# Performance work log

Measured on AMD Instinct MI355X. Metric: run time of the kernel, lower is better.

Reference implementation:

```python
import jax, jax.numpy as jnp
import numpy as np

NUM_NODES = 50000
NUM_EDGES = 800000
NUM_GRAPHS = 100
NODES_PER_GRAPH = 500
K = 250  # ceil(0.5 * NODES_PER_GRAPH), TopKPooling ratio=0.5
D = 64
OUT = 10


def gcn_conv(x, edge_index, W, b, num_nodes):
    """PyG GCNConv: add self-loops, symmetric D^-1/2 (A+I) D^-1/2 (x @ W) + b."""
    h = x @ W  # [N, Dout]
    loop = jnp.arange(num_nodes)
    row = jnp.concatenate([edge_index[0], loop])  # sources
    col = jnp.concatenate([edge_index[1], loop])  # targets
    deg = jax.ops.segment_sum(jnp.ones_like(col, dtype=h.dtype), col,
                              num_segments=num_nodes)
    dis = jnp.where(deg > 0, jax.lax.rsqrt(jnp.maximum(deg, 1e-12)), 0.0)
    norm = dis[row] * dis[col]                      # [E+N]
    msgs = h[row] * norm[:, None]                   # gather + scale (memory bound)
    out = jax.ops.segment_sum(msgs, col, num_segments=num_nodes)
    return out + b


def setup_inputs() -> dict:
    key = jax.random.key(0)
    ks = jax.random.split(key, 8)
    x = jax.random.normal(ks[0], (NUM_NODES, D), jnp.float32)
    edge_index = jax.random.randint(ks[1], (2, NUM_EDGES), 0, NUM_NODES)
    batch = jnp.arange(NUM_NODES) // NODES_PER_GRAPH  # contiguous equal graphs
    s = 1.0 / np.sqrt(D)
    W0 = jax.random.uniform(ks[2], (D, D), jnp.float32, -s, s)
    b0 = jnp.zeros((D,), jnp.float32)
    W1 = jax.random.uniform(ks[3], (D, D), jnp.float32, -s, s)
    b1 = jnp.zeros((D,), jnp.float32)
    pool_w = jax.random.uniform(ks[4], (D,), jnp.float32, -s, s)
    W_lin = jax.random.uniform(ks[5], (D, OUT), jnp.float32, -s, s)
    b_lin = jnp.zeros((OUT,), jnp.float32)
    return {"x": x, "edge_index": edge_index, "batch": batch,
            "W0": W0, "b0": b0, "W1": W1, "b1": b1,
            "pool_w": pool_w, "W_lin": W_lin, "b_lin": b_lin}


def reference(x, edge_index, batch, W0, b0, W1, b1, pool_w, W_lin, b_lin):
    # NOTE: zip(convs, pools) runs only 2 iterations -> 2 convs, 1 pool.
    x = jax.nn.relu(gcn_conv(x, edge_index, W0, b0, NUM_NODES))
    x = jax.nn.relu(gcn_conv(x, edge_index, W1, b1, NUM_NODES))
    # TopKPooling: score = tanh((x . w) / ||w||), keep top-K per graph,
    # kept features are scaled by their score.
    score = jnp.tanh((x @ pool_w) / jnp.linalg.norm(pool_w))  # [N]
    score_g = score.reshape(NUM_GRAPHS, NODES_PER_GRAPH)
    top_s, top_i = jax.lax.top_k(score_g, K)                  # [G, K]
    gidx = (top_i + jnp.arange(NUM_GRAPHS)[:, None] * NODES_PER_GRAPH).reshape(-1)
    x_pool = x[gidx] * top_s.reshape(-1, 1)                   # [G*K, D]
    # global_mean_pool: each pooled graph has exactly K nodes
    pooled = x_pool.reshape(NUM_GRAPHS, K, D).mean(axis=1)    # [G, D]
    logits = pooled @ W_lin + b_lin                           # [G, OUT]
    return jax.nn.log_softmax(logits, axis=1)
```

## Files before the change

kernel.cpp:

```cpp
#include <hip/hip_runtime.h>
#include <hip/hip_bf16.h>
#include <math.h>

#define NODES 50000
#define EDGES 800000
#define GRAPHS 100
#define NPG 500
#define KTOP 250
#define DIM 64
#define OUTC 10
#define SLOTS 64
#define GROWS 32
#define NBKT 196
#define BCAP 5120

#define WS_FLAG      0u
#define WS_INVNORM   4u
#define WS_W1F       512u
#define WS_B0F       16896u
#define WS_B1F       17152u
#define WS_PWF       17408u
#define WS_WLF       17664u
#define WS_BLF       20224u
#define WS_CURS      20480u
#define WS_CNT       21504u
#define WS_DIS       221696u
#define WS_SCORE     421888u
#define WS_EBUF      622080u
#define WS_SLOT      4636160u
#define WS_H1B       11036160u
#define WS_H2B       17436160u
#define WS_X2        23836160u
#define WS_A1B       WS_X2

__device__ __forceinline__ float bf16_bits_to_f32(unsigned short u) {
    return __uint_as_float(((unsigned int)u) << 16);
}
__device__ __forceinline__ float bf16_lo(unsigned int u) {
    return __uint_as_float(u << 16);
}
__device__ __forceinline__ float bf16_hi(unsigned int u) {
    return __uint_as_float(u & 0xffff0000u);
}
__device__ __forceinline__ unsigned short f32_to_bf16(float f) {
    unsigned int u = __float_as_uint(f);
    u += 0x7fffu + ((u >> 16) & 1u);
    return (unsigned short)(u >> 16);
}
__device__ __forceinline__ unsigned int f32_sortable(float f) {
    unsigned int b = __float_as_uint(f);
    return (b & 0x80000000u) ? ~b : (b | 0x80000000u);
}

__global__ __launch_bounds__(512) void k_bucket(const int* __restrict__ ei,
        const void* w0p, const void* b0p, const void* w1p, const void* b1p,
        const void* pwp, const void* wlp, const void* blp, char* __restrict__ ws) {
    int bid = blockIdx.x, t = threadIdx.x;
    if (bid < NBKT) {
        __shared__ int hist[NBKT];
        __shared__ int base[NBKT];
        if (t < NBKT) hist[t] = 0;
        __syncthreads();
        int e0 = bid * 4096;
        int rr[8], cc[8], loc[8];
        long be = (long)e0 + (long)t * 8;
        if (be + 8 <= EDGES) {
            int4 ra = ((const int4*)(ei + e0))[t * 2];
            int4 rb = ((const int4*)(ei + e0))[t * 2 + 1];
            int4 ca = ((const int4*)(ei + EDGES + e0))[t * 2];
            int4 cb = ((const int4*)(ei + EDGES + e0))[t * 2 + 1];
            rr[0] = ra.x; rr[1] = ra.y; rr[2] = ra.z; rr[3] = ra.w;
            rr[4] = rb.x; rr[5] = rb.y; rr[6] = rb.z; rr[7] = rb.w;
            cc[0] = ca.x; cc[1] = ca.y; cc[2] = ca.z; cc[3] = ca.w;
            cc[4] = cb.x; cc[5] = cb.y; cc[6] = cb.z; cc[7] = cb.w;
        } else {
#pragma unroll
            for (int j = 0; j < 8; j++) {
                long e = be + j;
                if (e < EDGES) { rr[j] = ei[e]; cc[j] = ei[EDGES + e]; }
                else cc[j] = -1;
            }
        }
#pragma unroll
        for (int j = 0; j < 8; j++)
            if (cc[j] >= 0) loc[j] = atomicAdd(&hist[cc[j] >> 8], 1);
        __syncthreads();
        if (t < NBKT) base[t] = atomicAdd((int*)(ws + WS_CURS) + t, hist[t]);
        __syncthreads();
        unsigned int* eb = (unsigned int*)(ws + WS_EBUF);
#pragma unroll
        for (int j = 0; j < 8; j++) {
            if (cc[j] >= 0) {
                int b = cc[j] >> 8;
                int o = base[b] + loc[j];
                if (o < BCAP)
                    eb[b * BCAP + o] =
                        ((unsigned int)(cc[j] & 255) << 16) | (unsigned int)rr[j];
            }
        }
        return;
    }
    __shared__ int red_sh[512];
    __shared__ float fred[64];
    const unsigned short* u16 = (const unsigned short*)w0p;
    int c = 0;
    for (int i = t; i < 4096; i += 512) {
        float v = bf16_bits_to_f32(u16[i]);
        float av = fabsf(v);
        if (v == 0.0f || (av >= 1e-9f && av <= 0.25f)) c++;
    }
    red_sh[t] = c;
    __syncthreads();
    for (int s = 256; s > 0; s >>= 1) {
        if (t < s) red_sh[t] += red_sh[t + s];
        __syncthreads();
    }
    int flag = (red_sh[0] >= 3686) ? 1 : 0;
    if (t == 0) *(int*)(ws + WS_FLAG) = flag;
    const void* srcs[6] = {w1p, b0p, b1p, pwp, wlp, blp};
    const int   ns[6]   = {4096, 64, 64, 64, 640, 10};
    const unsigned int dsts[6] = {WS_W1F, WS_B0F, WS_B1F, WS_PWF, WS_WLF, WS_BLF};
    for (int a = 0; a < 6; a++) {
        float* dst = (float*)(ws + dsts[a]);
        if (flag) {
            const unsigned short* sp = (const unsigned short*)srcs[a];
            for (int i = t; i < ns[a]; i += 512) dst[i] = bf16_bits_to_f32(sp[i]);
        } else {
            const float* sp = (const float*)srcs[a];
            for (int i = t; i < ns[a]; i += 512) dst[i] = sp[i];
        }
    }
    __syncthreads();
    if (t < 64) {
        float w = ((float*)(ws + WS_PWF))[t];
        fred[t] = w * w;
    }
    __syncthreads();
    if (t == 0) {
        float ssum = 0.f;
        for (int i = 0; i < 64; i++) ssum += fred[i];
        *(float*)(ws + WS_INVNORM) = rsqrtf(ssum);
    }
}

__global__ __launch_bounds__(1024) void k_build(char* __restrict__ ws) {
    int b = blockIdx.x, t = threadIdx.x;
    __shared__ int cl_cnt[256];
    if (t < 256) cl_cnt[t] = 0;
    __syncthreads();
    int n = ((const int*)(ws + WS_CURS))[b];
    if (n > BCAP) n = BCAP;
    const unsigned int* eb = (const unsigned int*)(ws + WS_EBUF) + b * BCAP;
    unsigned short* slot = (unsigned short*)(ws + WS_SLOT);
    for (int i = t; i < n; i += 1024) {
        unsigned int u = eb[i];
        int cl = u >> 16;
        int r = u & 0xffffu;
        int p = atomicAdd(&cl_cnt[cl], 1);
        if (p < SLOTS) slot[((b << 8) | cl) * SLOTS + p] = (unsigned short)r;
    }
    __syncthreads();
    if (t < 256) {
        int v = (b << 8) + t;
        if (v < NODES) {
            int cv = cl_cnt[t];
            ((int*)(ws + WS_CNT))[v] = cv;
            ((float*)(ws + WS_DIS))[v] = rsqrtf((float)(cv + 1));
        }
    }
}

__global__ __launch_bounds__(256) void k_gemm0(const void* __restrict__ xp,
        const void* __restrict__ w0p, char* __restrict__ ws,
        unsigned short* __restrict__ H1B) {
    __shared__ float Wsh[64 * 64];
    __shared__ float xsh[GROWS * 65];
    int bid = blockIdx.x, t = threadIdx.x;
    int flag = *(const int*)(ws + WS_FLAG);
    if (flag) {
        const unsigned short* wp = (const unsigned short*)w0p;
        for (int i = t; i < 4096; i += 256) Wsh[i] = bf16_bits_to_f32(wp[i]);
    } else {
        for (int i = t; i < 1024; i += 256)
            ((float4*)Wsh)[i] = ((const float4*)w0p)[i];
    }
    int row0 = bid * GROWS;
    for (int i = t; i < GROWS * 16; i += 256) {
        int r = i >> 4, q = i & 15;
        int gr = row0 + r;
        float4 v = {0.f, 0.f, 0.f, 0.f};
        if (gr < NODES) {
            if (flag) {
                ushort4 u = ((const ushort4*)xp)[gr * 16 + q];
                v.x = bf16_bits_to_f32(u.x); v.y = bf16_bits_to_f32(u.y);
                v.z = bf16_bits_to_f32(u.z); v.w = bf16_bits_to_f32(u.w);
            } else {
                v = ((const float4*)xp)[gr * 16 + q];
            }
        }
        float* xd = xsh + r * 65 + q * 4;
        xd[0] = v.x; xd[1] = v.y; xd[2] = v.z; xd[3] = v.w;
    }
    __syncthreads();
    int tc = t & 15, tr = t >> 4;
    int c0 = tc * 4, r0 = tr * 2;
    float4 a0 = {0, 0, 0, 0}, a1 = {0, 0, 0, 0};
#pragma unroll
    for (int k = 0; k < 64; k++) {
        float4 wv = *(const float4*)(Wsh + k * 64 + c0);
        float x0 = xsh[r0 * 65 + k];
        float x1 = xsh[(r0 + 1) * 65 + k];
        a0.x += wv.x * x0; a0.y += wv.y * x0; a0.z += wv.z * x0; a0.w += wv.w * x0;
        a1.x += wv.x * x1; a1.y += wv.y * x1; a1.z += wv.z * x1; a1.w += wv.w * x1;
    }
    int gr0 = row0 + r0;
    ushort4 s0, s1;
    s0.x = f32_to_bf16(a0.x); s0.y = f32_to_bf16(a0.y);
    s0.z = f32_to_bf16(a0.z); s0.w = f32_to_bf16(a0.w);
    s1.x = f32_to_bf16(a1.x); s1.y = f32_to_bf16(a1.y);
    s1.z = f32_to_bf16(a1.z); s1.w = f32_to_bf16(a1.w);
    if (gr0 < NODES)     *(ushort4*)(H1B + gr0 * 64 + c0) = s0;
    if (gr0 + 1 < NODES) *(ushort4*)(H1B + (gr0 + 1) * 64 + c0) = s1;
}

__global__ __launch_bounds__(256) void k_gemm1(const unsigned short* __restrict__ A1B,
        const char* __restrict__ ws, unsigned short* __restrict__ H2B) {
    __shared__ float Wsh[64 * 64];
    __shared__ float xsh[GROWS * 65];
    int bid = blockIdx.x, t = threadIdx.x;
    const float* W1F = (const float*)(ws + WS_W1F);
    for (int i = t; i < 1024; i += 256)
        ((float4*)Wsh)[i] = ((const float4*)W1F)[i];
    int row0 = bid * GROWS;
    for (int i = t; i < GROWS * 16; i += 256) {
        int r = i >> 4, q = i & 15;
        int gr = row0 + r;
        float4 v = {0.f, 0.f, 0.f, 0.f};
        if (gr < NODES) {
            ushort4 u = ((const ushort4*)A1B)[gr * 16 + q];
            v.x = bf16_bits_to_f32(u.x); v.y = bf16_bits_to_f32(u.y);
            v.z = bf16_bits_to_f32(u.z); v.w = bf16_bits_to_f32(u.w);
        }
        float* xd = xsh + r * 65 + q * 4;
        xd[0] = v.x; xd[1] = v.y; xd[2] = v.z; xd[3] = v.w;
    }
    __syncthreads();
    int tc = t & 15, tr = t >> 4;
    int c0 = tc * 4, r0 = tr * 2;
    float4 a0 = {0, 0, 0, 0}, a1 = {0, 0, 0, 0};
#pragma unroll
    for (int k = 0; k < 64; k++) {
        float4 wv = *(const float4*)(Wsh + k * 64 + c0);
        float x0 = xsh[r0 * 65 + k];
        float x1 = xsh[(r0 + 1) * 65 + k];
        a0.x += wv.x * x0; a0.y += wv.y * x0; a0.z += wv.z * x0; a0.w += wv.w * x0;
        a1.x += wv.x * x1; a1.y += wv.y * x1; a1.z += wv.z * x1; a1.w += wv.w * x1;
    }
    int gr0 = row0 + r0;
    ushort4 s0, s1;
    s0.x = f32_to_bf16(a0.x); s0.y = f32_to_bf16(a0.y);
    s0.z = f32_to_bf16(a0.z); s0.w = f32_to_bf16(a0.w);
    s1.x = f32_to_bf16(a1.x); s1.y = f32_to_bf16(a1.y);
    s1.z = f32_to_bf16(a1.z); s1.w = f32_to_bf16(a1.w);
    if (gr0 < NODES)     *(ushort4*)(H2B + gr0 * 64 + c0) = s0;
    if (gr0 + 1 < NODES) *(ushort4*)(H2B + (gr0 + 1) * 64 + c0) = s1;
}

__device__ __forceinline__ void agg_core(const unsigned short* __restrict__ HB,
        const char* __restrict__ ws, int v, int eg, int dh,
        const float* bias, float4& olo, float4& ohi) {
    const int* cnt = (const int*)(ws + WS_CNT);
    const unsigned short* slot = (const unsigned short*)(ws + WS_SLOT) + v * SLOTS;
    const float* dis = (const float*)(ws + WS_DIS);
    int deg = cnt[v];
    if (deg > SLOTS) deg = SLOTS;
    float dv = dis[v];
    float4 alo = {0, 0, 0, 0}, ahi = {0, 0, 0, 0};
    float4 blo = {0, 0, 0, 0}, bhi = {0, 0, 0, 0};
    if (eg == 0) {
        uint4 u = *(const uint4*)(HB + v * 64 + dh * 8);
        alo.x = bf16_lo(u.x) * dv; alo.y = bf16_hi(u.x) * dv;
        alo.z = bf16_lo(u.y) * dv; alo.w = bf16_hi(u.y) * dv;
        ahi.x = bf16_lo(u.z) * dv; ahi.y = bf16_hi(u.z) * dv;
        ahi.z = bf16_lo(u.w) * dv; ahi.w = bf16_hi(u.w) * dv;
    }
    int e = eg;
    for (; e + 8 < deg; e += 16) {
        int sA = slot[e], sB = slot[e + 8];
        float dA = dis[sA], dB = dis[sB];
        uint4 uA = *(const uint4*)(HB + sA * 64 + dh * 8);
        uint4 uB = *(const uint4*)(HB + sB * 64 + dh * 8);
        alo.x += bf16_lo(uA.x) * dA; alo.y += bf16_hi(uA.x) * dA;
        alo.z += bf16_lo(uA.y) * dA; alo.w += bf16_hi(uA.y) * dA;
        ahi.x += bf16_lo(uA.z) * dA; ahi.y += bf16_hi(uA.z) * dA;
        ahi.z += bf16_lo(uA.w) * dA; ahi.w += bf16_hi(uA.w) * dA;
        blo.x += bf16_lo(uB.x) * dB; blo.y += bf16_hi(uB.x) * dB;
        blo.z += bf16_lo(uB.y) * dB; blo.w += bf16_hi(uB.y) * dB;
        bhi.x += bf16_lo(uB.z) * dB; bhi.y += bf16_hi(uB.z) * dB;
        bhi.z += bf16_lo(uB.w) * dB; bhi.w += bf16_hi(uB.w) * dB;
    }
    if (e < deg) {
        int sA = slot[e];
        float dA = dis[sA];
        uint4 uA = *(const uint4*)(HB + sA * 64 + dh * 8);
        alo.x += bf16_lo(uA.x) * dA; alo.y += bf16_hi(uA.x) * dA;
        alo.z += bf16_lo(uA.y) * dA; alo.w += bf16_hi(uA.y) * dA;
        ahi.x += bf16_lo(uA.z) * dA; ahi.y += bf16_hi(uA.z) * dA;
        ahi.z += bf16_lo(uA.w) * dA; ahi.w += bf16_hi(uA.w) * dA;
    }
    alo.x += blo.x; alo.y += blo.y; alo.z += blo.z; alo.w += blo.w;
    ahi.x += bhi.x; ahi.y += bhi.y; ahi.z += bhi.z; ahi.w += bhi.w;
#pragma unroll
    for (int m = 8; m <= 32; m <<= 1) {
        alo.x += __shfl_xor(alo.x, m, 64); alo.y += __shfl_xor(alo.y, m, 64);
        alo.z += __shfl_xor(alo.z, m, 64); alo.w += __shfl_xor(alo.w, m, 64);
        ahi.x += __shfl_xor(ahi.x, m, 64); ahi.y += __shfl_xor(ahi.y, m, 64);
        ahi.z += __shfl_xor(ahi.z, m, 64); ahi.w += __shfl_xor(ahi.w, m, 64);
    }
    float4 b4a = *(const float4*)(bias + dh * 8);
    float4 b4b = *(const float4*)(bias + dh * 8 + 4);
    olo.x = fmaxf(alo.x * dv + b4a.x, 0.f);
    olo.y = fmaxf(alo.y * dv + b4a.y, 0.f);
    olo.z = fmaxf(alo.z * dv + b4a.z, 0.f);
    olo.w = fmaxf(alo.w * dv + b4a.w, 0.f);
    ohi.x = fmaxf(ahi.x * dv + b4b.x, 0.f);
    ohi.y = fmaxf(ahi.y * dv + b4b.y, 0.f);
    ohi.z = fmaxf(ahi.z * dv + b4b.z, 0.f);
    ohi.w = fmaxf(ahi.w * dv + b4b.w, 0.f);
}

__global__ __launch_bounds__(256) void k_agg1(const unsigned short* __restrict__ H1B,
        char* __restrict__ ws, unsigned short* __restrict__ A1B) {
    int t = threadIdx.x;
    int wv = t >> 6, lane = t & 63, eg = lane >> 3, dh = lane & 7;
    int v = blockIdx.x * 4 + wv;
    float4 olo, ohi;
    agg_core(H1B, ws, v, eg, dh, (const float*)(ws + WS_B0F), olo, ohi);
    if (eg == 0) {
        ushort4 s0, s1;
        s0.x = f32_to_bf16(olo.x); s0.y = f32_to_bf16(olo.y);
        s0.z = f32_to_bf16(olo.z); s0.w = f32_to_bf16(olo.w);
        s1.x = f32_to_bf16(ohi.x); s1.y = f32_to_bf16(ohi.y);
        s1.z = f32_to_bf16(ohi.z); s1.w = f32_to_bf16(ohi.w);
        *(ushort4*)(A1B + v * 64 + dh * 8) = s0;
        *(ushort4*)(A1B + v * 64 + dh * 8 + 4) = s1;
    }
}

__global__ __launch_bounds__(256) void k_agg_sc(const unsigned short* __restrict__ H2B,
        char* __restrict__ ws, float* __restrict__ X2) {
    int t = threadIdx.x;
    int wv = t >> 6, lane = t & 63, eg = lane >> 3, dh = lane & 7;
    int v = blockIdx.x * 4 + wv;
    float4 olo, ohi;
    agg_core(H2B, ws, v, eg, dh, (const float*)(ws + WS_B1F), olo, ohi);
    if (lane < 8) {
        *(float4*)(X2 + v * 64 + lane * 8) = olo;
        *(float4*)(X2 + v * 64 + lane * 8 + 4) = ohi;
    }
    const float* pw = (const float*)(ws + WS_PWF);
    float4 p4a = *(const float4*)(pw + dh * 8);
    float4 p4b = *(const float4*)(pw + dh * 8 + 4);
    float p = olo.x * p4a.x + olo.y * p4a.y + olo.z * p4a.z + olo.w * p4a.w
            + ohi.x * p4b.x + ohi.y * p4b.y + ohi.z * p4b.z + ohi.w * p4b.w;
    p += __shfl_xor(p, 1, 64);
    p += __shfl_xor(p, 2, 64);
    p += __shfl_xor(p, 4, 64);
    if (lane == 0) {
        float invn = *(const float*)(ws + WS_INVNORM);
        ((float*)(ws + WS_SCORE))[v] = tanhf(p * invn);
    }
}

template<int K, int J>
__device__ __forceinline__ void bstage(unsigned long long (&a)[8], int lane) {
    if constexpr (J >= 8) {
        constexpr int m = J >> 3;
#pragma unroll
        for (int s = 0; s < 8; s++) {
            unsigned long long other = __shfl_xor(a[s], m, 64);
            int e = (lane << 3) | s;
            bool keep_min = ((e & K) == 0) ^ ((lane & m) != 0);
            bool less = a[s] < other;
            a[s] = (keep_min == less) ? a[s] : other;
        }
    } else {
#pragma unroll
        for (int s = 0; s < 8; s++) {
            if ((s & J) == 0) {
                constexpr int j = J;
                int sp = s | j;
                int e = (lane << 3) | s;
                bool up = ((e & K) == 0);
                bool sw = up ? (a[s] > a[sp]) : (a[s] < a[sp]);
                if (sw) { unsigned long long tmp = a[s]; a[s] = a[sp]; a[sp] = tmp; }
            }
        }
    }
    if constexpr (J > 1) bstage<K, (J >> 1)>(a, lane);
}

__global__ __launch_bounds__(256) void k_topk(char* __restrict__ ws,
        const float* __restrict__ X2, void* __restrict__ out) {
    __shared__ unsigned long long pairs[KTOP];
    __shared__ float part[256];
    __shared__ float pool_sh[64];
    __shared__ float lsh[OUTC];
    int g = blockIdx.x, t = threadIdx.x;
    int wv = t >> 6, lane = t & 63;
    const float* sc = (const float*)(ws + WS_SCORE) + g * NPG;

    if (wv == 0) {
        unsigned long long a[8];
#pragma unroll
        for (int s = 0; s < 8; s++) {
            int e = (lane << 3) | s;
            if (e < NPG) {
                unsigned int key = ~f32_sortable(sc[e]);
                a[s] = ((unsigned long long)key << 32) | (unsigned int)e;
            } else {
                a[s] = 0xFFFFFFFFFFFFFFFFull;
            }
        }
        bstage<2, 1>(a, lane);
        bstage<4, 2>(a, lane);
        bstage<8, 4>(a, lane);
        bstage<16, 8>(a, lane);
        bstage<32, 16>(a, lane);
        bstage<64, 32>(a, lane);
        bstage<128, 64>(a, lane);
        bstage<256, 128>(a, lane);
        bstage<512, 256>(a, lane);
#pragma unroll
        for (int s = 0; s < 8; s++) {
            int r = (lane << 3) | s;
            if (r < KTOP) pairs[r] = a[s];
        }
    }
    __syncthreads();

    int d = lane;
    float acc = 0.f;
    for (int r = wv; r < KTOP; r += 4) {
        unsigned long long p = pairs[r];
        unsigned int u = ~(unsigned int)(p >> 32);
        unsigned int sbits = (u & 0x80000000u) ? (u ^ 0x80000000u) : ~u;
        float score = __uint_as_float(sbits);
        int idx = (int)(p & 0xFFFFFFFFu);
        acc += score * X2[(g * NPG + idx) * 64 + d];
    }
    part[t] = acc;
    __syncthreads();
    if (wv == 0)
        pool_sh[d] = (part[d] + part[64 + d] + part[128 + d] + part[192 + d]) * (1.0f / KTOP);
    __syncthreads();
    if (t < 64) {
        float pd = pool_sh[t];
        const float* Wl = (const float*)(ws + WS_WLF);
        const float* bl = (const float*)(ws + WS_BLF);
        for (int o = 0; o < OUTC; o++) {
            float p = pd * Wl[t * OUTC + o];
            for (int s = 32; s > 0; s >>= 1) p += __shfl_down(p, s, 64);
            if (t == 0) lsh[o] = p + bl[o];
        }
        if (t == 0) {
            int flag = *(const int*)(ws + WS_FLAG);
            float mx = lsh[0];
            for (int o = 1; o < OUTC; o++) mx = fmaxf(mx, lsh[o]);
            float se = 0.f;
            for (int o = 0; o < OUTC; o++) se += expf(lsh[o] - mx);
            float lse = logf(se);
            for (int o = 0; o < OUTC; o++) {
                float vv = lsh[o] - mx - lse;
                if (flag) ((__hip_bfloat16*)out)[g * OUTC + o] = __float2bfloat16(vv);
                else      ((float*)out)[g * OUTC + o] = vv;
            }
        }
    }
}

extern "C" void kernel_launch(void* const* d_in, const int* in_sizes, int n_in,
                              void* d_out, int out_size, void* d_ws, size_t ws_size,
                              hipStream_t stream) {
    (void)in_sizes; (void)n_in; (void)out_size; (void)ws_size;
    char* ws = (char*)d_ws;
    const void* xp = d_in[0];
    const int* ei = (const int*)d_in[1];
    unsigned short* H1B = (unsigned short*)(ws + WS_H1B);
    unsigned short* H2B = (unsigned short*)(ws + WS_H2B);
    unsigned short* A1B = (unsigned short*)(ws + WS_A1B);
    float* X2 = (float*)(ws + WS_X2);

    (void)hipMemsetAsync(ws + WS_CURS, 0, NBKT * sizeof(int), stream);
    k_bucket<<<NBKT + 1, 512, 0, stream>>>(ei, d_in[3], d_in[4], d_in[5],
                                           d_in[6], d_in[7], d_in[8], d_in[9], ws);
    k_build<<<NBKT, 1024, 0, stream>>>(ws);
    k_gemm0<<<1563, 256, 0, stream>>>(xp, d_in[3], ws, H1B);
    k_agg1<<<12500, 256, 0, stream>>>(H1B, ws, A1B);
    k_gemm1<<<1563, 256, 0, stream>>>(A1B, ws, H2B);
    k_agg_sc<<<12500, 256, 0, stream>>>(H2B, ws, X2);
    k_topk<<<100, 256, 0, stream>>>(ws, X2, d_out);
}
```

Measured before the change: 161.0 us.

## Fuse CSR build with first GEMM and fold second GEMM into aggregation

Merges the adjacency slot-building kernel and the first feature GEMM into one launch, with different block ranges doing independent work. The second GEMM is moved into the first aggregation kernel: each wave multiplies its aggregated row by an XOR-swizzled shared-memory copy of W1 and reduces across lanes with shuffles. This drops two launches and the write and read of the intermediate activation buffer. In exchange, every aggregation block reloads the 16 KB weight matrix, and the shuffle reduction adds extra work.

```diff
diff --git a/kernel.cpp b/kernel.cpp
--- a/kernel.cpp
+++ b/kernel.cpp
@@ -13,6 +13,7 @@
 #define GROWS 32
 #define NBKT 196
 #define BCAP 5120
+#define G0BLKS 782
 
 #define WS_FLAG      0u
 #define WS_INVNORM   4u
@@ -31,7 +32,6 @@
 #define WS_H1B       11036160u
 #define WS_H2B       17436160u
 #define WS_X2        23836160u
-#define WS_A1B       WS_X2
 
 __device__ __forceinline__ float bf16_bits_to_f32(unsigned short u) {
     return __uint_as_float(((unsigned int)u) << 16);
@@ -143,49 +143,51 @@
     }
 }
 
-__global__ __launch_bounds__(1024) void k_build(char* __restrict__ ws) {
-    int b = blockIdx.x, t = threadIdx.x;
-    __shared__ int cl_cnt[256];
-    if (t < 256) cl_cnt[t] = 0;
-    __syncthreads();
-    int n = ((const int*)(ws + WS_CURS))[b];
-    if (n > BCAP) n = BCAP;
-    const unsigned int* eb = (const unsigned int*)(ws + WS_EBUF) + b * BCAP;
-    unsigned short* slot = (unsigned short*)(ws + WS_SLOT);
-    for (int i = t; i < n; i += 1024) {
-        unsigned int u = eb[i];
-        int cl = u >> 16;
-        int r = u & 0xffffu;
-        int p = atomicAdd(&cl_cnt[cl], 1);
-        if (p < SLOTS) slot[((b << 8) | cl) * SLOTS + p] = (unsigned short)r;
-    }
-    __syncthreads();
-    if (t < 256) {
-        int v = (b << 8) + t;
-        if (v < NODES) {
-            int cv = cl_cnt[t];
-            ((int*)(ws + WS_CNT))[v] = cv;
-            ((float*)(ws + WS_DIS))[v] = rsqrtf((float)(cv + 1));
-        }
-    }
-}
-
-__global__ __launch_bounds__(256) void k_gemm0(const void* __restrict__ xp,
+__global__ __launch_bounds__(512) void k_build_g0(const void* __restrict__ xp,
         const void* __restrict__ w0p, char* __restrict__ ws,
         unsigned short* __restrict__ H1B) {
-    __shared__ float Wsh[64 * 64];
-    __shared__ float xsh[GROWS * 65];
-    int bid = blockIdx.x, t = threadIdx.x;
+    __shared__ float smem[4096 + 64 * 65];
+    int t = threadIdx.x;
+    if (blockIdx.x < NBKT) {
+        int b = blockIdx.x;
+        int* cl_cnt = (int*)smem;
+        if (t < 256) cl_cnt[t] = 0;
+        __syncthreads();
+        int n = ((const int*)(ws + WS_CURS))[b];
+        if (n > BCAP) n = BCAP;
+        const unsigned int* eb = (const unsigned int*)(ws + WS_EBUF) + b * BCAP;
+        unsigned short* slot = (unsigned short*)(ws + WS_SLOT);
+        for (int i = t; i < n; i += 512) {
+            unsigned int u = eb[i];
+            int cl = u >> 16;
+            int r = u & 0xffffu;
+            int p = atomicAdd(&cl_cnt[cl], 1);
+            if (p < SLOTS) slot[((b << 8) | cl) * SLOTS + p] = (unsigned short)r;
+        }
+        __syncthreads();
+        if (t < 256) {
+            int v = (b << 8) + t;
+            if (v < NODES) {
+                int cv = cl_cnt[t];
+                ((int*)(ws + WS_CNT))[v] = cv;
+                ((float*)(ws + WS_DIS))[v] = rsqrtf((float)(cv + 1));
+            }
+        }
+        return;
+    }
+    float* Wsh = smem;
+    float* xsh = smem + 4096;
+    int bid = blockIdx.x - NBKT;
     int flag = *(const int*)(ws + WS_FLAG);
     if (flag) {
         const unsigned short* wp = (const unsigned short*)w0p;
-        for (int i = t; i < 4096; i += 256) Wsh[i] = bf16_bits_to_f32(wp[i]);
+        for (int i = t; i < 4096; i += 512) Wsh[i] = bf16_bits_to_f32(wp[i]);
     } else {
-        for (int i = t; i < 1024; i += 256)
+        for (int i = t; i < 1024; i += 512)
             ((float4*)Wsh)[i] = ((const float4*)w0p)[i];
     }
-    int row0 = bid * GROWS;
-    for (int i = t; i < GROWS * 16; i += 256) {
+    int row0 = bid * 64;
+    for (int i = t; i < 64 * 16; i += 512) {
         int r = i >> 4, q = i & 15;
         int gr = row0 + r;
         float4 v = {0.f, 0.f, 0.f, 0.f};
@@ -221,49 +223,6 @@
     s1.z = f32_to_bf16(a1.z); s1.w = f32_to_bf16(a1.w);
     if (gr0 < NODES)     *(ushort4*)(H1B + gr0 * 64 + c0) = s0;
     if (gr0 + 1 < NODES) *(ushort4*)(H1B + (gr0 + 1) * 64 + c0) = s1;
-}
-
-__global__ __launch_bounds__(256) void k_gemm1(const unsigned short* __restrict__ A1B,
-        const char* __restrict__ ws, unsigned short* __restrict__ H2B) {
-    __shared__ float Wsh[64 * 64];
-    __shared__ float xsh[GROWS * 65];
-    int bid = blockIdx.x, t = threadIdx.x;
-    const float* W1F = (const float*)(ws + WS_W1F);
-    for (int i = t; i < 1024; i += 256)
-        ((float4*)Wsh)[i] = ((const float4*)W1F)[i];
-    int row0 = bid * GROWS;
-    for (int i = t; i < GROWS * 16; i += 256) {
-        int r = i >> 4, q = i & 15;
-        int gr = row0 + r;
-        float4 v = {0.f, 0.f, 0.f, 0.f};
-        if (gr < NODES) {
-            ushort4 u = ((const ushort4*)A1B)[gr * 16 + q];
-            v.x = bf16_bits_to_f32(u.x); v.y = bf16_bits_to_f32(u.y);
-            v.z = bf16_bits_to_f32(u.z); v.w = bf16_bits_to_f32(u.w);
-        }
-        float* xd = xsh + r * 65 + q * 4;
-        xd[0] = v.x; xd[1] = v.y; xd[2] = v.z; xd[3] = v.w;
-    }
-    __syncthreads();
-    int tc = t & 15, tr = t >> 4;
-    int c0 = tc * 4, r0 = tr * 2;
-    float4 a0 = {0, 0, 0, 0}, a1 = {0, 0, 0, 0};
-#pragma unroll
-    for (int k = 0; k < 64; k++) {
-        float4 wv = *(const float4*)(Wsh + k * 64 + c0);
-        float x0 = xsh[r0 * 65 + k];
-        float x1 = xsh[(r0 + 1) * 65 + k];
-        a0.x += wv.x * x0; a0.y += wv.y * x0; a0.z += wv.z * x0; a0.w += wv.w * x0;
-        a1.x += wv.x * x1; a1.y += wv.y * x1; a1.z += wv.z * x1; a1.w += wv.w * x1;
-    }
-    int gr0 = row0 + r0;
-    ushort4 s0, s1;
-    s0.x = f32_to_bf16(a0.x); s0.y = f32_to_bf16(a0.y);
-    s0.z = f32_to_bf16(a0.z); s0.w = f32_to_bf16(a0.w);
-    s1.x = f32_to_bf16(a1.x); s1.y = f32_to_bf16(a1.y);
-    s1.z = f32_to_bf16(a1.z); s1.w = f32_to_bf16(a1.w);
-    if (gr0 < NODES)     *(ushort4*)(H2B + gr0 * 64 + c0) = s0;
-    if (gr0 + 1 < NODES) *(ushort4*)(H2B + (gr0 + 1) * 64 + c0) = s1;
 }
 
 __device__ __forceinline__ void agg_core(const unsigned short* __restrict__ HB,
@@ -329,21 +288,49 @@
     ohi.w = fmaxf(ahi.w * dv + b4b.w, 0.f);
 }
 
-__global__ __launch_bounds__(256) void k_agg1(const unsigned short* __restrict__ H1B,
-        char* __restrict__ ws, unsigned short* __restrict__ A1B) {
+__global__ __launch_bounds__(512) void k_agg1g(const unsigned short* __restrict__ H1B,
+        char* __restrict__ ws, unsigned short* __restrict__ H2B) {
+    __shared__ float Wsh[4096];
     int t = threadIdx.x;
+    const float* W1F = (const float*)(ws + WS_W1F);
+    for (int i = t; i < 4096; i += 512) {
+        int k = i >> 6, cc = i & 63;
+        int qp = (cc >> 2) ^ (k >> 3);
+        Wsh[k * 64 + (qp << 2) + (cc & 3)] = W1F[i];
+    }
+    __syncthreads();
     int wv = t >> 6, lane = t & 63, eg = lane >> 3, dh = lane & 7;
-    int v = blockIdx.x * 4 + wv;
+    int v = blockIdx.x * 8 + wv;
     float4 olo, ohi;
     agg_core(H1B, ws, v, eg, dh, (const float*)(ws + WS_B0F), olo, ohi);
-    if (eg == 0) {
-        ushort4 s0, s1;
-        s0.x = f32_to_bf16(olo.x); s0.y = f32_to_bf16(olo.y);
-        s0.z = f32_to_bf16(olo.z); s0.w = f32_to_bf16(olo.w);
-        s1.x = f32_to_bf16(ohi.x); s1.y = f32_to_bf16(ohi.y);
-        s1.z = f32_to_bf16(ohi.z); s1.w = f32_to_bf16(ohi.w);
-        *(ushort4*)(A1B + v * 64 + dh * 8) = s0;
-        *(ushort4*)(A1B + v * 64 + dh * 8 + 4) = s1;
+    float av[8] = {olo.x, olo.y, olo.z, olo.w, ohi.x, ohi.y, ohi.z, ohi.w};
+    float y[8] = {0.f, 0.f, 0.f, 0.f, 0.f, 0.f, 0.f, 0.f};
+    const float* Wk = Wsh + dh * 512;
+    int q0 = (((eg << 1)) ^ dh) << 2;
+    int q1 = (((eg << 1) | 1) ^ dh) << 2;
+#pragma unroll
+    for (int j = 0; j < 8; j++) {
+        float a = av[j];
+        float4 w0 = *(const float4*)(Wk + j * 64 + q0);
+        float4 w1 = *(const float4*)(Wk + j * 64 + q1);
+        y[0] += a * w0.x; y[1] += a * w0.y; y[2] += a * w0.z; y[3] += a * w0.w;
+        y[4] += a * w1.x; y[5] += a * w1.y; y[6] += a * w1.z; y[7] += a * w1.w;
+    }
+#pragma unroll
+    for (int m = 1; m <= 4; m <<= 1) {
+#pragma unroll
+        for (int q = 0; q < 8; q++) y[q] += __shfl_xor(y[q], m, 64);
+    }
+    if (dh < 2) {
+        ushort4 s;
+        if (dh == 0) {
+            s.x = f32_to_bf16(y[0]); s.y = f32_to_bf16(y[1]);
+            s.z = f32_to_bf16(y[2]); s.w = f32_to_bf16(y[3]);
+        } else {
+            s.x = f32_to_bf16(y[4]); s.y = f32_to_bf16(y[5]);
+            s.z = f32_to_bf16(y[6]); s.w = f32_to_bf16(y[7]);
+        }
+        *(ushort4*)(H2B + v * 64 + (eg << 3) + (dh << 2)) = s;
     }
 }
 
@@ -488,16 +475,13 @@
     const int* ei = (const int*)d_in[1];
     unsigned short* H1B = (unsigned short*)(ws + WS_H1B);
     unsigned short* H2B = (unsigned short*)(ws + WS_H2B);
-    unsigned short* A1B = (unsigned short*)(ws + WS_A1B);
     float* X2 = (float*)(ws + WS_X2);
 
     (void)hipMemsetAsync(ws + WS_CURS, 0, NBKT * sizeof(int), stream);
     k_bucket<<<NBKT + 1, 512, 0, stream>>>(ei, d_in[3], d_in[4], d_in[5],
                                            d_in[6], d_in[7], d_in[8], d_in[9], ws);
-    k_build<<<NBKT, 1024, 0, stream>>>(ws);
-    k_gemm0<<<1563, 256, 0, stream>>>(xp, d_in[3], ws, H1B);
-    k_agg1<<<12500, 256, 0, stream>>>(H1B, ws, A1B);
-    k_gemm1<<<1563, 256, 0, stream>>>(A1B, ws, H2B);
+    k_build_g0<<<NBKT + G0BLKS, 512, 0, stream>>>(xp, d_in[3], ws, H1B);
+    k_agg1g<<<6250, 512, 0, stream>>>(H1B, ws, H2B);
     k_agg_sc<<<12500, 256, 0, stream>>>(H2B, ws, X2);
     k_topk<<<100, 256, 0, stream>>>(ws, X2, d_out);
 }
```

New measurement: 198.4 us. +23.2%, slower.
